# Optimization experiments

Hardware: AMD Instinct MI355X
Metric: run time of the kernel (lower is better)

Reference implementation:

```python
import jax, jax.numpy as jnp
import numpy as np

D_MODEL = 1024
N_HEADS = 16
D_K = D_MODEL // N_HEADS
B, L = 2, 2048


def setup_inputs() -> dict:
    key = jax.random.key(0)
    ks = jax.random.split(key, 13)
    s = 0.02
    inp = {
        'query': jax.random.normal(ks[0], (B, L, D_MODEL), jnp.float32),
        'key': jax.random.normal(ks[1], (B, L, D_MODEL), jnp.float32),
        'value': jax.random.normal(ks[2], (B, L, D_MODEL), jnp.float32),
        'mask': jax.random.randint(ks[3], (1, 1, L, L), 0, 2).astype(bool),
        'W_q': jax.random.normal(ks[4], (D_MODEL, D_MODEL), jnp.float32) * s,
        'b_q': jnp.zeros((D_MODEL,), jnp.float32),
        'W_k': jax.random.normal(ks[5], (D_MODEL, D_MODEL), jnp.float32) * s,
        'b_k': jnp.zeros((D_MODEL,), jnp.float32),
        'W_v': jax.random.normal(ks[6], (D_MODEL, D_MODEL), jnp.float32) * s,
        'b_v': jnp.zeros((D_MODEL,), jnp.float32),
        'W_o': jax.random.normal(ks[7], (D_MODEL, D_MODEL), jnp.float32) * s,
        'b_o': jnp.zeros((D_MODEL,), jnp.float32),
    }
    return inp


def _split_heads(x):
    b, l, _ = x.shape
    return x.reshape(b, l, N_HEADS, D_K).transpose(0, 2, 1, 3)  # [B,H,L,dk]


def reference(query, key, value, mask, W_q, b_q, W_k, b_k, W_v, b_v, W_o, b_o):
    q = _split_heads(query @ W_q + b_q)
    k = _split_heads(key @ W_k + b_k)
    v = _split_heads(value @ W_v + b_v)
    # Unscaled attention logits [B,H,L,L] (NO 1/sqrt(dk))
    logits = jnp.einsum('bhqd,bhkd->bhqk', q, k)
    logits = jnp.where(mask, -jnp.inf, logits)
    w = jax.nn.softmax(logits, axis=-1)
    w = jnp.nan_to_num(w, nan=0.0)  # fully-masked rows -> zeros
    attended = jnp.einsum('bhqk,bhkd->bhqd', w, v)
    # dropout in eval mode = identity; combine heads
    out = attended.transpose(0, 2, 1, 3).reshape(B, L, D_MODEL)
    return out @ W_o + b_o
```

## Files before the change

### kernel.cpp

```cpp
#include <hip/hip_runtime.h>
#include <hip/hip_bf16.h>
#include <stdint.h>


typedef __bf16 bf16;
typedef __bf16 bf16x8 __attribute__((ext_vector_type(8)));
typedef float f32x4 __attribute__((ext_vector_type(4)));

#define AS1 __attribute__((address_space(1)))
#define AS3 __attribute__((address_space(3)))

__device__ __forceinline__ void g2l16(const void* g, void* l) {
    __builtin_amdgcn_global_load_lds((AS1 void*)g, (AS3 void*)l, 16, 0, 0);
}

__device__ __forceinline__ bool lane_masked(unsigned long long m) {
#if __has_builtin(__builtin_amdgcn_inverse_ballot_w64)
    return __builtin_amdgcn_inverse_ballot_w64(m);
#else
    return (m >> (threadIdx.x & 63)) & 1ull;
#endif
}

#define LOG2E 1.44269504088896f

__global__ __launch_bounds__(256) void cvt3_kernel(const float* __restrict__ a0,
                                                   const float* __restrict__ a1,
                                                   const float* __restrict__ a2,
                                                   bf16* o0, bf16* o1, bf16* o2) {
    int y = blockIdx.y;
    const float* in = (y == 0) ? a0 : (y == 1) ? a1 : a2;
    bf16* out = (y == 0) ? o0 : (y == 1) ? o1 : o2;
    int idx = blockIdx.x * 256 + threadIdx.x;
    float4 v = ((const float4*)in)[idx];
    __align__(8) bf16 o[4];
    o[0] = (bf16)v.x; o[1] = (bf16)v.y; o[2] = (bf16)v.z; o[3] = (bf16)v.w;
    *(uint2*)(out + (size_t)idx * 4) = *(const uint2*)o;
}

__global__ __launch_bounds__(256) void mdetect_kernel(const unsigned int* __restrict__ w,
                                                      int* __restrict__ flag) {
    int idx = blockIdx.x * 256 + threadIdx.x;
    unsigned v = w[idx];
    int f = 0;
    if (v == 0x3F800000u) f = 2;
    else if (v > 1u) f = 1;
    unsigned long long b1 = __ballot(f & 1);
    unsigned long long b2 = __ballot(f & 2);
    if ((threadIdx.x & 63) == 0) {
        int agg = (b1 ? 1 : 0) | (b2 ? 2 : 0);
        if (agg) atomicOr(flag, agg);
    }
}

__global__ __launch_bounds__(256) void mpack_kernel(const void* __restrict__ mask,
                                                    unsigned long long* __restrict__ mb,
                                                    const int* __restrict__ flag) {
    int idx = blockIdx.x * 256 + threadIdx.x;
    int f = *flag;
    bool v;
    if (f & 2)      v = ((const float*)mask)[idx] != 0.0f;
    else if (f & 1) v = ((const unsigned char*)mask)[idx] != 0;
    else            v = ((const int*)mask)[idx] != 0;
    unsigned long long b = __ballot(v);
    if ((threadIdx.x & 63) == 0) mb[idx >> 6] = b;
}

__global__ __launch_bounds__(256) void rpack_kernel(const unsigned long long* __restrict__ mb,
                                                    unsigned long long* __restrict__ rmb) {
    int task = blockIdx.x * 4 + (threadIdx.x >> 6);
    int qg = task >> 5, kt = task & 31;
    int lane = threadIdx.x & 63, quad = lane >> 4, col = lane & 15;
    #pragma unroll
    for (int r = 0; r < 4; ++r) {
        unsigned long long wrow = mb[(size_t)(qg * 16 + quad * 4 + r) * 32 + kt];
        #pragma unroll
        for (int nt = 0; nt < 4; ++nt) {
            unsigned long long b = __ballot(((wrow >> (nt * 16 + col)) & 1ull) != 0);
            if (lane == 0) rmb[(size_t)task * 16 + r * 4 + nt] = b;
        }
    }
}

__global__ __launch_bounds__(256) void wtrans_kernel(const float* W0, const float* W1,
                                                     const float* W2, const float* W3,
                                                     bf16* T0, bf16* T1, bf16* T2, bf16* T3) {
    const float* W; bf16* T;
    int y = blockIdx.y;
    if (y == 0)      { W = W0; T = T0; }
    else if (y == 1) { W = W1; T = T1; }
    else if (y == 2) { W = W2; T = T2; }
    else             { W = W3; T = T3; }
    int tx = blockIdx.x & 15, ty = blockIdx.x >> 4;
    int n0 = tx * 64, k0 = ty * 64;
    __shared__ __align__(16) bf16 t[64 * 72];
    int tid = threadIdx.x;
    #pragma unroll
    for (int rr = 0; rr < 4; ++rr) {
        int idx = rr * 256 + tid;
        int r = idx >> 4, c4 = (idx & 15) * 4;
        float4 v = *(const float4*)(W + (size_t)(k0 + r) * 1024 + n0 + c4);
        __align__(8) bf16 o[4];
        o[0] = (bf16)v.x; o[1] = (bf16)v.y; o[2] = (bf16)v.z; o[3] = (bf16)v.w;
        *(uint2*)&t[r * 72 + c4] = *(const uint2*)o;
    }
    __syncthreads();
    #pragma unroll
    for (int rr = 0; rr < 2; ++rr) {
        int idx = rr * 256 + tid;
        int n = idx >> 3, kc = (idx & 7) * 8;
        __align__(16) bf16 o[8];
        #pragma unroll
        for (int j = 0; j < 8; ++j) o[j] = t[(kc + j) * 72 + n];
        *(uint4*)(T + (size_t)(n0 + n) * 1024 + k0 + kc) = *(const uint4*)o;
    }
}

template <int MODE>
__device__ __forceinline__ void gemm128_core(const bf16* __restrict__ A,
                                             const bf16* __restrict__ Bt,
                                             const float* __restrict__ bias,
                                             void* __restrict__ Out, int bm, int bn,
                                             float scale) {
    __shared__ __align__(16) bf16 la[128 * 32];
    __shared__ __align__(16) bf16 lb[128 * 32];
    int tid = threadIdx.x;
    int w = tid >> 6, lane = tid & 63;
    int quad = lane >> 4, col = lane & 15;
    int wm = w >> 1, wn = w & 1;
    int m0 = bm * 128, n0 = bn * 128;
    f32x4 acc[4][4];
    f32x4 z = {0.f, 0.f, 0.f, 0.f};
    #pragma unroll
    for (int i = 0; i < 4; ++i)
        #pragma unroll
        for (int j = 0; j < 4; ++j) acc[i][j] = z;
    int srow = lane >> 2;
    int skc = (lane & 3) * 8;
    for (int kt = 0; kt < 32; ++kt) {
        int kk = kt * 32;
        __syncthreads();
        #pragma unroll
        for (int rr = 0; rr < 2; ++rr) {
            int ch = rr * 4 + w;
            int row = ch * 16 + srow;
            g2l16(A + (size_t)(m0 + row) * 1024 + kk + skc, &la[ch * 512]);
            g2l16(Bt + (size_t)(n0 + row) * 1024 + kk + skc, &lb[ch * 512]);
        }
        __syncthreads();
        bf16x8 af[4], bfr[4];
        #pragma unroll
        for (int mt = 0; mt < 4; ++mt)
            af[mt] = *(const bf16x8*)&la[(wm * 64 + mt * 16 + col) * 32 + quad * 8];
        #pragma unroll
        for (int nt = 0; nt < 4; ++nt)
            bfr[nt] = *(const bf16x8*)&lb[(wn * 64 + nt * 16 + col) * 32 + quad * 8];
        #pragma unroll
        for (int mt = 0; mt < 4; ++mt)
            #pragma unroll
            for (int nt = 0; nt < 4; ++nt)
                acc[mt][nt] = __builtin_amdgcn_mfma_f32_16x16x32_bf16(
                    af[mt], bfr[nt], acc[mt][nt], 0, 0, 0);
    }
    float bia[4];
    #pragma unroll
    for (int nt = 0; nt < 4; ++nt) bia[nt] = bias[n0 + wn * 64 + nt * 16 + col];
    #pragma unroll
    for (int mt = 0; mt < 4; ++mt) {
        #pragma unroll
        for (int nt = 0; nt < 4; ++nt) {
            #pragma unroll
            for (int r = 0; r < 4; ++r) {
                int m = m0 + wm * 64 + mt * 16 + quad * 4 + r;
                int n = n0 + wn * 64 + nt * 16 + col;
                float v = (acc[mt][nt][r] + bia[nt]) * scale;
                if (MODE == 0) {
                    int b = m >> 11, l = m & 2047, h = n >> 6, d = n & 63;
                    ((bf16*)Out)[(((size_t)b * 16 + h) * 2048 + l) * 64 + d] = (bf16)v;
                } else {
                    int b = m >> 11, l = m & 2047, h = n >> 6, d = n & 63;
                    ((bf16*)Out)[(((size_t)b * 16 + h) * 64 + d) * 2048 + l] = (bf16)v;
                }
            }
        }
    }
}

__global__ __launch_bounds__(256) void qkv_kernel(
    const bf16* Xq, const bf16* Xk, const bf16* Xv,
    const bf16* Wq, const bf16* Wk, const bf16* Wv,
    const float* bq, const float* bk, const float* bv,
    bf16* Qh, bf16* Kh, bf16* Vt) {
    int y = blockIdx.y;
    int bm = blockIdx.x >> 3, bn = blockIdx.x & 7;
    if (y == 0)      gemm128_core<0>(Xq, Wq, bq, Qh, bm, bn, LOG2E);
    else if (y == 1) gemm128_core<0>(Xk, Wk, bk, Kh, bm, bn, 1.0f);
    else             gemm128_core<2>(Xv, Wv, bv, Vt, bm, bn, 1.0f);
}

__global__ __launch_bounds__(256) void ogemm_kernel(const bf16* __restrict__ A,
                                                    const bf16* __restrict__ Wt,
                                                    const float* __restrict__ bias,
                                                    float* __restrict__ Out) {
    int bm = blockIdx.x >> 3, bn = blockIdx.x & 7;
    __shared__ __align__(16) bf16 la[64 * 32];
    __shared__ __align__(16) bf16 lb[128 * 32];
    int tid = threadIdx.x;
    int w = tid >> 6, lane = tid & 63;
    int quad = lane >> 4, col = lane & 15;
    int m0 = bm * 64, n0 = bn * 128;
    f32x4 acc[4][2];
    f32x4 z = {0.f, 0.f, 0.f, 0.f};
    #pragma unroll
    for (int i = 0; i < 4; ++i) { acc[i][0] = z; acc[i][1] = z; }
    int srow = lane >> 2;
    int skc = (lane & 3) * 8;
    for (int kt = 0; kt < 32; ++kt) {
        int kk = kt * 32;
        __syncthreads();
        g2l16(A + (size_t)(m0 + w * 16 + srow) * 1024 + kk + skc, &la[w * 512]);
        #pragma unroll
        for (int rr = 0; rr < 2; ++rr) {
            int ch = rr * 4 + w;
            g2l16(Wt + (size_t)(n0 + ch * 16 + srow) * 1024 + kk + skc, &lb[ch * 512]);
        }
        __syncthreads();
        bf16x8 af[4], bfr[2];
        #pragma unroll
        for (int mt = 0; mt < 4; ++mt)
            af[mt] = *(const bf16x8*)&la[(mt * 16 + col) * 32 + quad * 8];
        #pragma unroll
        for (int nt = 0; nt < 2; ++nt)
            bfr[nt] = *(const bf16x8*)&lb[(w * 32 + nt * 16 + col) * 32 + quad * 8];
        #pragma unroll
        for (int mt = 0; mt < 4; ++mt)
            #pragma unroll
            for (int nt = 0; nt < 2; ++nt)
                acc[mt][nt] = __builtin_amdgcn_mfma_f32_16x16x32_bf16(
                    af[mt], bfr[nt], acc[mt][nt], 0, 0, 0);
    }
    float bia[2];
    bia[0] = bias[n0 + w * 32 + col];
    bia[1] = bias[n0 + w * 32 + 16 + col];
    #pragma unroll
    for (int mt = 0; mt < 4; ++mt)
        #pragma unroll
        for (int nt = 0; nt < 2; ++nt)
            #pragma unroll
            for (int r = 0; r < 4; ++r)
                Out[(size_t)(m0 + mt * 16 + quad * 4 + r) * 1024 +
                    n0 + w * 32 + nt * 16 + col] = acc[mt][nt][r] + bia[nt];
}

__global__ __launch_bounds__(128) void attn_kernel(const bf16* __restrict__ Qh,
                                                   const bf16* __restrict__ Kh,
                                                   const bf16* __restrict__ Vt,
                                                   const unsigned long long* __restrict__ rmb,
                                                   bf16* __restrict__ att) {
    int bh = blockIdx.x, qt = blockIdx.y;
    int b = bh >> 4, h = bh & 15;
    int q0 = qt * 64;
    __shared__ __align__(16) bf16 ks[64 * 64];
    __shared__ __align__(16) bf16 vs[64 * 64];
    __shared__ __align__(16) bf16 ps[2 * 32 * 72];
    int tid = threadIdx.x;
    int w = tid >> 6, lane = tid & 63;
    int quad = lane >> 4, col = lane & 15;
    int c7 = col & 7;
    int sr = lane >> 3;
    int sg = (lane & 7) ^ sr;
    int swz0 = (quad ^ c7) * 8;
    int swz1 = ((4 + quad) ^ c7) * 8;

    int mofs = __builtin_amdgcn_readfirstlane((qt * 4 + w * 2) * 512);

    #pragma unroll
    for (int i = 0; i < 4; ++i) {
        int ch = w * 4 + i;
        g2l16(Qh + ((size_t)bh * 2048 + q0 + ch * 8 + sr) * 64 + sg * 8, &ks[ch * 512]);
    }
    __syncthreads();
    bf16x8 aq[2][2];
    #pragma unroll
    for (int mt = 0; mt < 2; ++mt) {
        aq[mt][0] = *(const bf16x8*)&ks[(w * 32 + mt * 16 + col) * 64 + swz0];
        aq[mt][1] = *(const bf16x8*)&ks[(w * 32 + mt * 16 + col) * 64 + swz1];
    }
    bf16x8 onesf;
    #pragma unroll
    for (int i = 0; i < 8; ++i) onesf[i] = (bf16)1.0f;

    f32x4 z = {0.f, 0.f, 0.f, 0.f};
    f32x4 O[2][4], R[2];
    #pragma unroll
    for (int mt = 0; mt < 2; ++mt) {
        R[mt] = z;
        #pragma unroll
        for (int i = 0; i < 4; ++i) O[mt][i] = z;
    }

    for (int kt = 0; kt < 32; ++kt) {
        __syncthreads();
        #pragma unroll
        for (int i = 0; i < 4; ++i) {
            int ch = w * 4 + i;
            int r = ch * 8 + sr;
            g2l16(Kh + ((size_t)bh * 2048 + kt * 64 + r) * 64 + sg * 8, &ks[ch * 512]);
            g2l16(Vt + ((size_t)bh * 64 + r) * 2048 + kt * 64 + sg * 8, &vs[ch * 512]);
        }
        __syncthreads();

        f32x4 s[2][4];
        #pragma unroll
        for (int nt = 0; nt < 4; ++nt) {
            s[0][nt] = z; s[1][nt] = z;
            bf16x8 bk0 = *(const bf16x8*)&ks[(nt * 16 + col) * 64 + swz0];
            s[0][nt] = __builtin_amdgcn_mfma_f32_16x16x32_bf16(aq[0][0], bk0, s[0][nt], 0, 0, 0);
            s[1][nt] = __builtin_amdgcn_mfma_f32_16x16x32_bf16(aq[1][0], bk0, s[1][nt], 0, 0, 0);
            bf16x8 bk1 = *(const bf16x8*)&ks[(nt * 16 + col) * 64 + swz1];
            s[0][nt] = __builtin_amdgcn_mfma_f32_16x16x32_bf16(aq[0][1], bk1, s[0][nt], 0, 0, 0);
            s[1][nt] = __builtin_amdgcn_mfma_f32_16x16x32_bf16(aq[1][1], bk1, s[1][nt], 0, 0, 0);
        }

        #pragma unroll
        for (int mt = 0; mt < 2; ++mt) {
            const unsigned long long* mw = rmb + mofs + mt * 512 + kt * 16;
            #pragma unroll
            for (int r = 0; r < 4; ++r) {
                #pragma unroll
                for (int nt = 0; nt < 4; ++nt) {
                    float p = __builtin_amdgcn_exp2f(s[mt][nt][r]);
                    if (lane_masked(mw[r * 4 + nt])) p = 0.0f;
                    ps[w * 2304 + (mt * 16 + quad * 4 + r) * 72 + nt * 16 + col] = (bf16)p;
                }
            }
        }

        bf16x8 ap[2][2];
        #pragma unroll
        for (int mt = 0; mt < 2; ++mt) {
            ap[mt][0] = *(const bf16x8*)&ps[w * 2304 + (mt * 16 + col) * 72 + quad * 8];
            ap[mt][1] = *(const bf16x8*)&ps[w * 2304 + (mt * 16 + col) * 72 + 32 + quad * 8];
        }
        #pragma unroll
        for (int dt = 0; dt < 4; ++dt) {
            bf16x8 bv0 = *(const bf16x8*)&vs[(dt * 16 + col) * 64 + swz0];
            O[0][dt] = __builtin_amdgcn_mfma_f32_16x16x32_bf16(ap[0][0], bv0, O[0][dt], 0, 0, 0);
            O[1][dt] = __builtin_amdgcn_mfma_f32_16x16x32_bf16(ap[1][0], bv0, O[1][dt], 0, 0, 0);
            bf16x8 bv1 = *(const bf16x8*)&vs[(dt * 16 + col) * 64 + swz1];
            O[0][dt] = __builtin_amdgcn_mfma_f32_16x16x32_bf16(ap[0][1], bv1, O[0][dt], 0, 0, 0);
            O[1][dt] = __builtin_amdgcn_mfma_f32_16x16x32_bf16(ap[1][1], bv1, O[1][dt], 0, 0, 0);
        }
        #pragma unroll
        for (int mt = 0; mt < 2; ++mt) {
            R[mt] = __builtin_amdgcn_mfma_f32_16x16x32_bf16(ap[mt][0], onesf, R[mt], 0, 0, 0);
            R[mt] = __builtin_amdgcn_mfma_f32_16x16x32_bf16(ap[mt][1], onesf, R[mt], 0, 0, 0);
        }
    }

    #pragma unroll
    for (int mt = 0; mt < 2; ++mt) {
        #pragma unroll
        for (int r = 0; r < 4; ++r) {
            float rsv = R[mt][r];
            float inv = (rsv > 0.f) ? 1.0f / rsv : 0.f;
            int qg = q0 + w * 32 + mt * 16 + quad * 4 + r;
            #pragma unroll
            for (int dt = 0; dt < 4; ++dt) {
                float ov = O[mt][dt][r] * inv;
                att[((size_t)b * 2048 + qg) * 1024 + h * 64 + dt * 16 + col] = (bf16)ov;
            }
        }
    }
}

extern "C" void kernel_launch(void* const* d_in, const int* in_sizes, int n_in,
                              void* d_out, int out_size, void* d_ws, size_t ws_size,
                              hipStream_t stream) {
    (void)in_sizes; (void)n_in; (void)out_size; (void)ws_size;
    const float* query = (const float*)d_in[0];
    const float* key_  = (const float*)d_in[1];
    const float* value = (const float*)d_in[2];
    const void*  mask  = d_in[3];
    const float* W_q = (const float*)d_in[4];
    const float* b_q = (const float*)d_in[5];
    const float* W_k = (const float*)d_in[6];
    const float* b_k = (const float*)d_in[7];
    const float* W_v = (const float*)d_in[8];
    const float* b_v = (const float*)d_in[9];
    const float* W_o = (const float*)d_in[10];
    const float* b_o = (const float*)d_in[11];

    char* ws = (char*)d_ws;
    bf16* Xq  = (bf16*)(ws + 0);
    bf16* Xk  = (bf16*)(ws + 8388608);
    bf16* Xv  = (bf16*)(ws + 16777216);
    bf16* Wtq = (bf16*)(ws + 25165824);
    bf16* Wtk = (bf16*)(ws + 27262976);
    bf16* Wtv = (bf16*)(ws + 29360128);
    bf16* Wto = (bf16*)(ws + 31457280);
    bf16* Qh  = (bf16*)(ws + 33554432);
    bf16* Kh  = (bf16*)(ws + 41943040);
    bf16* Vt  = (bf16*)(ws + 50331648);
    bf16* att = (bf16*)(ws + 58720256);
    unsigned long long* mb  = (unsigned long long*)(ws + 67108864);
    unsigned long long* rmb = (unsigned long long*)(ws + 67633152);
    int* flag = (int*)(ws + 68157440);

    hipMemsetAsync(flag, 0, 4, stream);
    mdetect_kernel<<<4096, 256, 0, stream>>>((const unsigned int*)mask, flag);
    mpack_kernel<<<16384, 256, 0, stream>>>(mask, mb, flag);
    rpack_kernel<<<1024, 256, 0, stream>>>(mb, rmb);

    cvt3_kernel<<<dim3(4096, 3), 256, 0, stream>>>(query, key_, value, Xq, Xk, Xv);
    wtrans_kernel<<<dim3(256, 4), 256, 0, stream>>>(W_q, W_k, W_v, W_o, Wtq, Wtk, Wtv, Wto);

    qkv_kernel<<<dim3(256, 3), 256, 0, stream>>>(Xq, Xk, Xv, Wtq, Wtk, Wtv,
                                                 b_q, b_k, b_v, Qh, Kh, Vt);
    attn_kernel<<<dim3(32, 32), 128, 0, stream>>>(Qh, Kh, Vt, rmb, att);
    ogemm_kernel<<<512, 256, 0, stream>>>(att, Wto, b_o, (float*)d_out);
}
```

Baseline: 274.3 us.

## Software-pipeline attention loop: overlap QK of next tile with softmax-PV of previous

Restructures the attention key loop so each iteration computes QK^T for the current K tile while running the masked exp and PV MFMAs on the previous tile's scores. V is double-buffered in LDS so the previous V tile stays available. The P scratch buffer also drops its padding in favour of an XOR swizzle to avoid LDS bank conflicts. This aims to hide MFMA and exp latency through extra independent work, at the cost of more registers and LDS, which may reduce occupancy.

Measured after the change: 298.0 us. 1.09x slower.

```diff
diff --git a/kernel.cpp b/kernel.cpp
--- a/kernel.cpp
+++ b/kernel.cpp
@@ -261,8 +261,9 @@
     int b = bh >> 4, h = bh & 15;
     int q0 = qt * 64;
     __shared__ __align__(16) bf16 ks[64 * 64];
-    __shared__ __align__(16) bf16 vs[64 * 64];
-    __shared__ __align__(16) bf16 ps[2 * 32 * 72];
+    __shared__ __align__(16) bf16 vsA[64 * 64];
+    __shared__ __align__(16) bf16 vsB[64 * 64];
+    __shared__ __align__(16) bf16 ps[2][32 * 64];
     int tid = threadIdx.x;
     int w = tid >> 6, lane = tid & 63;
     int quad = lane >> 4, col = lane & 15;
@@ -298,19 +299,18 @@
         #pragma unroll
         for (int i = 0; i < 4; ++i) O[mt][i] = z;
     }
-
-    for (int kt = 0; kt < 32; ++kt) {
-        __syncthreads();
+    f32x4 sA[2][4], sB[2][4];
+
+    auto stage = [&](int t, bf16* vdst) {
         #pragma unroll
         for (int i = 0; i < 4; ++i) {
             int ch = w * 4 + i;
             int r = ch * 8 + sr;
-            g2l16(Kh + ((size_t)bh * 2048 + kt * 64 + r) * 64 + sg * 8, &ks[ch * 512]);
-            g2l16(Vt + ((size_t)bh * 64 + r) * 2048 + kt * 64 + sg * 8, &vs[ch * 512]);
-        }
-        __syncthreads();
-
-        f32x4 s[2][4];
+            g2l16(Kh + ((size_t)bh * 2048 + t * 64 + r) * 64 + sg * 8, &ks[ch * 512]);
+            g2l16(Vt + ((size_t)bh * 64 + r) * 2048 + t * 64 + sg * 8, vdst + ch * 512);
+        }
+    };
+    auto qk = [&](f32x4 (&s)[2][4]) {
         #pragma unroll
         for (int nt = 0; nt < 4; ++nt) {
             s[0][nt] = z; s[1][nt] = z;
@@ -321,33 +321,35 @@
             s[0][nt] = __builtin_amdgcn_mfma_f32_16x16x32_bf16(aq[0][1], bk1, s[0][nt], 0, 0, 0);
             s[1][nt] = __builtin_amdgcn_mfma_f32_16x16x32_bf16(aq[1][1], bk1, s[1][nt], 0, 0, 0);
         }
-
+    };
+    auto smpv = [&](f32x4 (&s)[2][4], const bf16* vsrc, int tp) {
         #pragma unroll
         for (int mt = 0; mt < 2; ++mt) {
-            const unsigned long long* mw = rmb + mofs + mt * 512 + kt * 16;
+            const unsigned long long* mw = rmb + mofs + mt * 512 + tp * 16;
             #pragma unroll
             for (int r = 0; r < 4; ++r) {
+                int row = mt * 16 + quad * 4 + r;
+                int xs = ((quad * 4 + r) & 7) << 3;
                 #pragma unroll
                 for (int nt = 0; nt < 4; ++nt) {
                     float p = __builtin_amdgcn_exp2f(s[mt][nt][r]);
                     if (lane_masked(mw[r * 4 + nt])) p = 0.0f;
-                    ps[w * 2304 + (mt * 16 + quad * 4 + r) * 72 + nt * 16 + col] = (bf16)p;
+                    ps[w][row * 64 + ((nt * 16 + col) ^ xs)] = (bf16)p;
                 }
             }
         }
-
         bf16x8 ap[2][2];
         #pragma unroll
         for (int mt = 0; mt < 2; ++mt) {
-            ap[mt][0] = *(const bf16x8*)&ps[w * 2304 + (mt * 16 + col) * 72 + quad * 8];
-            ap[mt][1] = *(const bf16x8*)&ps[w * 2304 + (mt * 16 + col) * 72 + 32 + quad * 8];
+            ap[mt][0] = *(const bf16x8*)&ps[w][(mt * 16 + col) * 64 + swz0];
+            ap[mt][1] = *(const bf16x8*)&ps[w][(mt * 16 + col) * 64 + swz1];
         }
         #pragma unroll
         for (int dt = 0; dt < 4; ++dt) {
-            bf16x8 bv0 = *(const bf16x8*)&vs[(dt * 16 + col) * 64 + swz0];
+            bf16x8 bv0 = *(const bf16x8*)&vsrc[(dt * 16 + col) * 64 + swz0];
             O[0][dt] = __builtin_amdgcn_mfma_f32_16x16x32_bf16(ap[0][0], bv0, O[0][dt], 0, 0, 0);
             O[1][dt] = __builtin_amdgcn_mfma_f32_16x16x32_bf16(ap[1][0], bv0, O[1][dt], 0, 0, 0);
-            bf16x8 bv1 = *(const bf16x8*)&vs[(dt * 16 + col) * 64 + swz1];
+            bf16x8 bv1 = *(const bf16x8*)&vsrc[(dt * 16 + col) * 64 + swz1];
             O[0][dt] = __builtin_amdgcn_mfma_f32_16x16x32_bf16(ap[0][1], bv1, O[0][dt], 0, 0, 0);
             O[1][dt] = __builtin_amdgcn_mfma_f32_16x16x32_bf16(ap[1][1], bv1, O[1][dt], 0, 0, 0);
         }
@@ -356,7 +358,27 @@
             R[mt] = __builtin_amdgcn_mfma_f32_16x16x32_bf16(ap[mt][0], onesf, R[mt], 0, 0, 0);
             R[mt] = __builtin_amdgcn_mfma_f32_16x16x32_bf16(ap[mt][1], onesf, R[mt], 0, 0, 0);
         }
-    }
+    };
+    auto step = [&](int t, f32x4 (&cur)[2][4], f32x4 (&prev)[2][4],
+                    bf16* vcur, const bf16* vprev) {
+        __syncthreads();
+        stage(t, vcur);
+        __syncthreads();
+        qk(cur);
+        smpv(prev, vprev, t - 1);
+    };
+
+    __syncthreads();
+    stage(0, vsA);
+    __syncthreads();
+    qk(sA);
+
+    for (int p = 0; p < 15; ++p) {
+        step(2 * p + 1, sB, sA, vsB, vsA);
+        step(2 * p + 2, sA, sB, vsA, vsB);
+    }
+    step(31, sB, sA, vsB, vsA);
+    smpv(sB, vsB, 31);
 
     #pragma unroll
     for (int mt = 0; mt < 2; ++mt) {
```

## Double GEMM K-tile to 64 with XOR-swizzled LDS, merge prep kernels

Applied to the files above, without the earlier changes.

Both the QKV and output-projection GEMMs now stage 64-wide K tiles instead of 32. This halves the number of loop iterations and barrier pairs. The LDS layout uses an XOR swizzle on 16-byte groups so that fragment reads avoid bank conflicts. The input conversion and weight transpose kernels are merged into one launch to remove a kernel launch, at the cost of many early-exiting blocks in the weight section. Doubling the LDS footprint may reduce occupancy.

Result: no change. 279.7 us (+2.0%).

```diff
diff --git a/kernel.cpp b/kernel.cpp
--- a/kernel.cpp
+++ b/kernel.cpp
@@ -23,20 +23,6 @@
 }
 
 #define LOG2E 1.44269504088896f
-
-__global__ __launch_bounds__(256) void cvt3_kernel(const float* __restrict__ a0,
-                                                   const float* __restrict__ a1,
-                                                   const float* __restrict__ a2,
-                                                   bf16* o0, bf16* o1, bf16* o2) {
-    int y = blockIdx.y;
-    const float* in = (y == 0) ? a0 : (y == 1) ? a1 : a2;
-    bf16* out = (y == 0) ? o0 : (y == 1) ? o1 : o2;
-    int idx = blockIdx.x * 256 + threadIdx.x;
-    float4 v = ((const float4*)in)[idx];
-    __align__(8) bf16 o[4];
-    o[0] = (bf16)v.x; o[1] = (bf16)v.y; o[2] = (bf16)v.z; o[3] = (bf16)v.w;
-    *(uint2*)(out + (size_t)idx * 4) = *(const uint2*)o;
-}
 
 __global__ __launch_bounds__(256) void mdetect_kernel(const unsigned int* __restrict__ w,
                                                       int* __restrict__ flag) {
@@ -82,26 +68,42 @@
     }
 }
 
-__global__ __launch_bounds__(256) void wtrans_kernel(const float* W0, const float* W1,
-                                                     const float* W2, const float* W3,
-                                                     bf16* T0, bf16* T1, bf16* T2, bf16* T3) {
+__global__ __launch_bounds__(256) void prep_kernel(
+    const float* __restrict__ q, const float* __restrict__ k, const float* __restrict__ v,
+    bf16* xq, bf16* xk, bf16* xv,
+    const float* W0, const float* W1, const float* W2, const float* W3,
+    bf16* T0, bf16* T1, bf16* T2, bf16* T3) {
+    __shared__ __align__(16) bf16 t[64 * 72];
+    int y = blockIdx.y;
+    int tid = threadIdx.x;
+    if (y < 3) {
+        const float* in = (y == 0) ? q : (y == 1) ? k : v;
+        bf16* out = (y == 0) ? xq : (y == 1) ? xk : xv;
+        int idx = blockIdx.x * 256 + tid;
+        float4 vv = ((const float4*)in)[idx];
+        __align__(8) bf16 o[4];
+        o[0] = (bf16)vv.x; o[1] = (bf16)vv.y; o[2] = (bf16)vv.z; o[3] = (bf16)vv.w;
+        *(uint2*)(out + (size_t)idx * 4) = *(const uint2*)o;
+        return;
+    }
+    int bx = blockIdx.x;
+    if (bx >= 1024) return;
     const float* W; bf16* T;
-    int y = blockIdx.y;
-    if (y == 0)      { W = W0; T = T0; }
-    else if (y == 1) { W = W1; T = T1; }
-    else if (y == 2) { W = W2; T = T2; }
-    else             { W = W3; T = T3; }
-    int tx = blockIdx.x & 15, ty = blockIdx.x >> 4;
+    int wi = bx >> 8;
+    if (wi == 0)      { W = W0; T = T0; }
+    else if (wi == 1) { W = W1; T = T1; }
+    else if (wi == 2) { W = W2; T = T2; }
+    else              { W = W3; T = T3; }
+    int x = bx & 255;
+    int tx = x & 15, ty = x >> 4;
     int n0 = tx * 64, k0 = ty * 64;
-    __shared__ __align__(16) bf16 t[64 * 72];
-    int tid = threadIdx.x;
     #pragma unroll
     for (int rr = 0; rr < 4; ++rr) {
         int idx = rr * 256 + tid;
         int r = idx >> 4, c4 = (idx & 15) * 4;
-        float4 v = *(const float4*)(W + (size_t)(k0 + r) * 1024 + n0 + c4);
+        float4 vv = *(const float4*)(W + (size_t)(k0 + r) * 1024 + n0 + c4);
         __align__(8) bf16 o[4];
-        o[0] = (bf16)v.x; o[1] = (bf16)v.y; o[2] = (bf16)v.z; o[3] = (bf16)v.w;
+        o[0] = (bf16)vv.x; o[1] = (bf16)vv.y; o[2] = (bf16)vv.z; o[3] = (bf16)vv.w;
         *(uint2*)&t[r * 72 + c4] = *(const uint2*)o;
     }
     __syncthreads();
@@ -122,11 +124,12 @@
                                              const float* __restrict__ bias,
                                              void* __restrict__ Out, int bm, int bn,
                                              float scale) {
-    __shared__ __align__(16) bf16 la[128 * 32];
-    __shared__ __align__(16) bf16 lb[128 * 32];
+    __shared__ __align__(16) bf16 la[128 * 64];
+    __shared__ __align__(16) bf16 lb[128 * 64];
     int tid = threadIdx.x;
     int w = tid >> 6, lane = tid & 63;
     int quad = lane >> 4, col = lane & 15;
+    int c7 = col & 7;
     int wm = w >> 1, wn = w & 1;
     int m0 = bm * 128, n0 = bn * 128;
     f32x4 acc[4][4];
@@ -135,32 +138,41 @@
     for (int i = 0; i < 4; ++i)
         #pragma unroll
         for (int j = 0; j < 4; ++j) acc[i][j] = z;
-    int srow = lane >> 2;
-    int skc = (lane & 3) * 8;
-    for (int kt = 0; kt < 32; ++kt) {
-        int kk = kt * 32;
-        __syncthreads();
-        #pragma unroll
-        for (int rr = 0; rr < 2; ++rr) {
-            int ch = rr * 4 + w;
-            int row = ch * 16 + srow;
-            g2l16(A + (size_t)(m0 + row) * 1024 + kk + skc, &la[ch * 512]);
-            g2l16(Bt + (size_t)(n0 + row) * 1024 + kk + skc, &lb[ch * 512]);
-        }
-        __syncthreads();
-        bf16x8 af[4], bfr[4];
+    int sr = lane >> 3;
+    int sg = (lane & 7) ^ sr;
+    int swz0 = (quad ^ c7) * 8;
+    int swz1 = ((4 + quad) ^ c7) * 8;
+    for (int kt = 0; kt < 16; ++kt) {
+        int kk = kt * 64;
+        __syncthreads();
+        #pragma unroll
+        for (int i = 0; i < 4; ++i) {
+            int ch = w * 4 + i;
+            int row = ch * 8 + sr;
+            g2l16(A + (size_t)(m0 + row) * 1024 + kk + sg * 8, &la[ch * 512]);
+            g2l16(Bt + (size_t)(n0 + row) * 1024 + kk + sg * 8, &lb[ch * 512]);
+        }
+        __syncthreads();
+        bf16x8 af[4][2], bfr[4][2];
+        #pragma unroll
+        for (int mt = 0; mt < 4; ++mt) {
+            af[mt][0] = *(const bf16x8*)&la[(wm * 64 + mt * 16 + col) * 64 + swz0];
+            af[mt][1] = *(const bf16x8*)&la[(wm * 64 + mt * 16 + col) * 64 + swz1];
+        }
+        #pragma unroll
+        for (int nt = 0; nt < 4; ++nt) {
+            bfr[nt][0] = *(const bf16x8*)&lb[(wn * 64 + nt * 16 + col) * 64 + swz0];
+            bfr[nt][1] = *(const bf16x8*)&lb[(wn * 64 + nt * 16 + col) * 64 + swz1];
+        }
         #pragma unroll
         for (int mt = 0; mt < 4; ++mt)
-            af[mt] = *(const bf16x8*)&la[(wm * 64 + mt * 16 + col) * 32 + quad * 8];
-        #pragma unroll
-        for (int nt = 0; nt < 4; ++nt)
-            bfr[nt] = *(const bf16x8*)&lb[(wn * 64 + nt * 16 + col) * 32 + quad * 8];
-        #pragma unroll
-        for (int mt = 0; mt < 4; ++mt)
-            #pragma unroll
-            for (int nt = 0; nt < 4; ++nt)
+            #pragma unroll
+            for (int nt = 0; nt < 4; ++nt) {
                 acc[mt][nt] = __builtin_amdgcn_mfma_f32_16x16x32_bf16(
-                    af[mt], bfr[nt], acc[mt][nt], 0, 0, 0);
+                    af[mt][0], bfr[nt][0], acc[mt][nt], 0, 0, 0);
+                acc[mt][nt] = __builtin_amdgcn_mfma_f32_16x16x32_bf16(
+                    af[mt][1], bfr[nt][1], acc[mt][nt], 0, 0, 0);
+            }
     }
     float bia[4];
     #pragma unroll
@@ -203,41 +215,55 @@
                                                     const float* __restrict__ bias,
                                                     float* __restrict__ Out) {
     int bm = blockIdx.x >> 3, bn = blockIdx.x & 7;
-    __shared__ __align__(16) bf16 la[64 * 32];
-    __shared__ __align__(16) bf16 lb[128 * 32];
+    __shared__ __align__(16) bf16 la[64 * 64];
+    __shared__ __align__(16) bf16 lb[128 * 64];
     int tid = threadIdx.x;
     int w = tid >> 6, lane = tid & 63;
     int quad = lane >> 4, col = lane & 15;
+    int c7 = col & 7;
     int m0 = bm * 64, n0 = bn * 128;
     f32x4 acc[4][2];
     f32x4 z = {0.f, 0.f, 0.f, 0.f};
     #pragma unroll
     for (int i = 0; i < 4; ++i) { acc[i][0] = z; acc[i][1] = z; }
-    int srow = lane >> 2;
-    int skc = (lane & 3) * 8;
-    for (int kt = 0; kt < 32; ++kt) {
-        int kk = kt * 32;
-        __syncthreads();
-        g2l16(A + (size_t)(m0 + w * 16 + srow) * 1024 + kk + skc, &la[w * 512]);
-        #pragma unroll
-        for (int rr = 0; rr < 2; ++rr) {
-            int ch = rr * 4 + w;
-            g2l16(Wt + (size_t)(n0 + ch * 16 + srow) * 1024 + kk + skc, &lb[ch * 512]);
-        }
-        __syncthreads();
-        bf16x8 af[4], bfr[2];
+    int sr = lane >> 3;
+    int sg = (lane & 7) ^ sr;
+    int swz0 = (quad ^ c7) * 8;
+    int swz1 = ((4 + quad) ^ c7) * 8;
+    for (int kt = 0; kt < 16; ++kt) {
+        int kk = kt * 64;
+        __syncthreads();
+        #pragma unroll
+        for (int i = 0; i < 2; ++i) {
+            int ch = w * 2 + i;
+            g2l16(A + (size_t)(m0 + ch * 8 + sr) * 1024 + kk + sg * 8, &la[ch * 512]);
+        }
+        #pragma unroll
+        for (int i = 0; i < 4; ++i) {
+            int ch = w * 4 + i;
+            g2l16(Wt + (size_t)(n0 + ch * 8 + sr) * 1024 + kk + sg * 8, &lb[ch * 512]);
+        }
+        __syncthreads();
+        bf16x8 af[4][2], bfr[2][2];
+        #pragma unroll
+        for (int mt = 0; mt < 4; ++mt) {
+            af[mt][0] = *(const bf16x8*)&la[(mt * 16 + col) * 64 + swz0];
+            af[mt][1] = *(const bf16x8*)&la[(mt * 16 + col) * 64 + swz1];
+        }
+        #pragma unroll
+        for (int nt = 0; nt < 2; ++nt) {
+            bfr[nt][0] = *(const bf16x8*)&lb[(w * 32 + nt * 16 + col) * 64 + swz0];
+            bfr[nt][1] = *(const bf16x8*)&lb[(w * 32 + nt * 16 + col) * 64 + swz1];
+        }
         #pragma unroll
         for (int mt = 0; mt < 4; ++mt)
-            af[mt] = *(const bf16x8*)&la[(mt * 16 + col) * 32 + quad * 8];
-        #pragma unroll
-        for (int nt = 0; nt < 2; ++nt)
-            bfr[nt] = *(const bf16x8*)&lb[(w * 32 + nt * 16 + col) * 32 + quad * 8];
-        #pragma unroll
-        for (int mt = 0; mt < 4; ++mt)
-            #pragma unroll
-            for (int nt = 0; nt < 2; ++nt)
+            #pragma unroll
+            for (int nt = 0; nt < 2; ++nt) {
                 acc[mt][nt] = __builtin_amdgcn_mfma_f32_16x16x32_bf16(
-                    af[mt], bfr[nt], acc[mt][nt], 0, 0, 0);
+                    af[mt][0], bfr[nt][0], acc[mt][nt], 0, 0, 0);
+                acc[mt][nt] = __builtin_amdgcn_mfma_f32_16x16x32_bf16(
+                    af[mt][1], bfr[nt][1], acc[mt][nt], 0, 0, 0);
+            }
     }
     float bia[2];
     bia[0] = bias[n0 + w * 32 + col];
@@ -412,8 +438,9 @@
     mpack_kernel<<<16384, 256, 0, stream>>>(mask, mb, flag);
     rpack_kernel<<<1024, 256, 0, stream>>>(mb, rmb);
 
-    cvt3_kernel<<<dim3(4096, 3), 256, 0, stream>>>(query, key_, value, Xq, Xk, Xv);
-    wtrans_kernel<<<dim3(256, 4), 256, 0, stream>>>(W_q, W_k, W_v, W_o, Wtq, Wtk, Wtv, Wto);
+    prep_kernel<<<dim3(4096, 4), 256, 0, stream>>>(query, key_, value, Xq, Xk, Xv,
+                                                   W_q, W_k, W_v, W_o,
+                                                   Wtq, Wtk, Wtv, Wto);
 
     qkv_kernel<<<dim3(256, 3), 256, 0, stream>>>(Xq, Xk, Xv, Wtq, Wtk, Wtv,
                                                  b_q, b_k, b_v, Qh, Kh, Vt);
```
